# Performance work log

Hardware: AMD Instinct MI355X
Metric: run time of the kernel (lower is better)

The kernel has to match this reference:

```python
import jax, jax.numpy as jnp
import numpy as np

B, L, D = 2, 2048, 2048
H = 16
DH = D // H  # 128
EPS = 1e-6


def _rope_cos_sin(seq_len, dim, dtype):
    inv_freq = 1.0 / (10000.0 ** (jnp.arange(0, dim, 2, dtype=jnp.float32) / dim))
    t = jnp.arange(seq_len, dtype=jnp.float32)
    freqs = jnp.einsum('i,j->ij', t, inv_freq)          # [L, dim/2]
    emb = jnp.concatenate([freqs, freqs], axis=-1)      # [L, dim]
    return jnp.cos(emb).astype(dtype)[None, None], jnp.sin(emb).astype(dtype)[None, None]


def _rotate_half(x):
    x1, x2 = jnp.split(x, 2, axis=-1)
    return jnp.concatenate([-x2, x1], axis=-1)


def _rms_norm(x, w):
    var = jnp.mean(jnp.square(x), axis=-1, keepdims=True)
    return x * jax.lax.rsqrt(var + EPS) * w


def setup_inputs() -> dict:
    key = jax.random.key(0)
    ks = jax.random.split(key, 4)
    s_in = 1.0 / np.sqrt(D)
    return {
        'x': jax.random.normal(ks[0], (B, L, D), jnp.float32),
        'attention_mask': jnp.zeros((B, 1, 1, L), jnp.bool_),
        'Wqkv': jax.random.normal(ks[1], (D, 3 * D), jnp.float32) * s_in,
        'bqkv': jnp.zeros((3 * D,), jnp.float32),
        'Wout': jax.random.normal(ks[2], (D, D), jnp.float32) * s_in,
        'bout': jnp.zeros((D,), jnp.float32),
        'q_norm_w': jnp.ones((DH,), jnp.float32),
        'k_norm_w': jnp.ones((DH,), jnp.float32),
    }


def reference(x, attention_mask, Wqkv, bqkv, Wout, bout, q_norm_w, k_norm_w):
    b, l, d = x.shape
    qkv = x @ Wqkv + bqkv                                   # [B,L,3D]
    q, k, v = jnp.split(qkv, 3, axis=-1)
    # [B,H,L,DH]
    q = q.reshape(b, l, H, DH).transpose(0, 2, 1, 3)
    k = k.reshape(b, l, H, DH).transpose(0, 2, 1, 3)
    v = v.reshape(b, l, H, DH).transpose(0, 2, 1, 3)

    cos, sin = _rope_cos_sin(l, DH, x.dtype)
    q = q * cos + _rotate_half(q) * sin
    k = k * cos + _rotate_half(k) * sin

    q = _rms_norm(q, q_norm_w)
    k = _rms_norm(k, k_norm_w)

    # SDPA with additive (float-cast) mask, as in the original code
    scale = 1.0 / np.sqrt(DH)
    scores = jnp.einsum('bhqd,bhkd->bhqk', q, k) * scale
    scores = scores + attention_mask.astype(x.dtype)        # broadcast [B,1,1,L]
    attn = jax.nn.softmax(scores, axis=-1)
    out = jnp.einsum('bhqk,bhkd->bhqd', attn, v)            # [B,H,L,DH]

    # zero out masked query rows: padding_mask = mask.transpose(2,3) -> [B,1,L,1]
    padding_mask = jnp.swapaxes(attention_mask, 2, 3)
    out = jnp.where(padding_mask, 0.0, out)

    out = out.transpose(0, 2, 1, 3).reshape(b, l, d)
    return out @ Wout + bout
```

## Files before the change

kernel.cpp:

```cpp
#include <hip/hip_runtime.h>
#include <hip/hip_bf16.h>

typedef __bf16 bf16;
using bf16x8 = __attribute__((ext_vector_type(8))) __bf16;
using bf16x4 = __attribute__((ext_vector_type(4))) __bf16;
using f32x4  = __attribute__((ext_vector_type(4))) float;
using f32x16 = __attribute__((ext_vector_type(16))) float;

#define DEV __device__ __forceinline__

DEV void load_lds16(const void* g, void* l) {
  __builtin_amdgcn_global_load_lds(
      (const __attribute__((address_space(1))) void*)g,
      (__attribute__((address_space(3))) void*)l, 16, 0, 0);
}

__global__ void k_tab(float* __restrict__ invf) {
  int i = threadIdx.x;
  invf[i] = 1.0f / (float)pow(10000.0, (double)i / 64.0);
}

__global__ void k_f2b(const float* __restrict__ in, bf16* __restrict__ out, long n) {
  long i = ((long)blockIdx.x * blockDim.x + threadIdx.x) * 8;
  if (i >= n) return;
  float4 a = *(const float4*)(in + i);
  float4 b = *(const float4*)(in + i + 4);
  bf16x8 o;
  o[0] = (bf16)a.x; o[1] = (bf16)a.y; o[2] = (bf16)a.z; o[3] = (bf16)a.w;
  o[4] = (bf16)b.x; o[5] = (bf16)b.y; o[6] = (bf16)b.z; o[7] = (bf16)b.w;
  *(bf16x8*)(out + i) = o;
}

__global__ __launch_bounds__(256) void k_tconv(const float* __restrict__ in,
                                               bf16* __restrict__ out, int R, int C) {
  __shared__ float t[64][65];
  int nbc = C >> 6;
  long r0 = (long)(blockIdx.x / nbc) * 64, c0 = (long)(blockIdx.x % nbc) * 64;
  int tid = threadIdx.x;
#pragma unroll
  for (int i = 0; i < 4; ++i) {
    int ch = tid + i * 256;
    int r = ch >> 4, c4 = (ch & 15) * 4;
    float4 v = *(const float4*)(in + (r0 + r) * C + c0 + c4);
    t[r][c4] = v.x; t[r][c4 + 1] = v.y; t[r][c4 + 2] = v.z; t[r][c4 + 3] = v.w;
  }
  __syncthreads();
#pragma unroll
  for (int i = 0; i < 2; ++i) {
    int ch = tid + i * 256;
    int c = ch >> 3, r8 = (ch & 7) * 8;
    bf16x8 o;
#pragma unroll
    for (int j = 0; j < 8; ++j) o[j] = (bf16)t[r8 + j][c];
    *(bf16x8*)(out + (c0 + c) * R + r0 + r8) = o;
  }
}

template <typename OutT>
__global__ __launch_bounds__(256) void k_gemm_bt(
    const bf16* __restrict__ A, const bf16* __restrict__ Bt,
    const float* __restrict__ bias, OutT* __restrict__ C,
    int M, int N, int K, int fuse,
    const float* __restrict__ invf,
    const float* __restrict__ qw, const float* __restrict__ kw,
    bf16* __restrict__ q_r, bf16* __restrict__ k_r, bf16* __restrict__ v_t) {
  __shared__ __align__(16) bf16 lAB[2][128 * 64];
  bf16* lA = lAB[0];
  bf16* lB = lAB[1];
  int bid = blockIdx.x;
  if ((gridDim.x & 7) == 0) {
    int q = gridDim.x >> 3;
    bid = (bid & 7) * q + (bid >> 3);
  }
  int nbn = N >> 7;
  int bm = bid / nbn, bn = bid % nbn;
  const int tid = threadIdx.x, lane = tid & 63, wid = tid >> 6;
  const int wr = wid >> 1, wc = wid & 1;
  const int fr = lane & 15, fq = lane >> 4;
  const long abase = (long)bm * 128 * K, bbase = (long)bn * 128 * K;
  f32x4 acc[4][4] = {};

  for (int k0 = 0; k0 < K; k0 += 64) {
    __syncthreads();
#pragma unroll
    for (int it = 0; it < 4; ++it) {
      int ch = it * 256 + tid;
      int r = ch >> 3, u = ch & 7;
      load_lds16(A + abase + (long)r * K + k0 + ((u ^ (r & 7)) << 3), &lA[ch * 8]);
    }
#pragma unroll
    for (int it = 0; it < 4; ++it) {
      int ch = it * 256 + tid;
      int r = ch >> 3, u = ch & 7;
      load_lds16(Bt + bbase + (long)r * K + k0 + ((u ^ (r & 7)) << 3), &lB[ch * 8]);
    }
    __syncthreads();
    bf16x8 af[4][2], bf_[4][2];
#pragma unroll
    for (int m = 0; m < 4; ++m) {
      int R = wr * 64 + m * 16 + fr;
#pragma unroll
      for (int kk = 0; kk < 2; ++kk)
        af[m][kk] = *(const bf16x8*)&lA[R * 64 + (((kk * 4 + fq) ^ (R & 7)) << 3)];
    }
#pragma unroll
    for (int n = 0; n < 4; ++n) {
      int R = wc * 64 + n * 16 + fr;
#pragma unroll
      for (int kk = 0; kk < 2; ++kk)
        bf_[n][kk] = *(const bf16x8*)&lB[R * 64 + (((kk * 4 + fq) ^ (R & 7)) << 3)];
    }
#pragma unroll
    for (int m = 0; m < 4; ++m)
#pragma unroll
      for (int n = 0; n < 4; ++n)
#pragma unroll
        for (int kk = 0; kk < 2; ++kk)
          acc[m][n] = __builtin_amdgcn_mfma_f32_16x16x32_bf16(af[m][kk], bf_[n][kk],
                                                              acc[m][n], 0, 0, 0);
  }

  if (!fuse) {
#pragma unroll
    for (int n = 0; n < 4; ++n) {
      int col = bn * 128 + wc * 64 + n * 16 + fr;
      float bv = bias[col];
#pragma unroll
      for (int m = 0; m < 4; ++m) {
        int row0 = bm * 128 + wr * 64 + m * 16 + fq * 4;
#pragma unroll
        for (int r = 0; r < 4; ++r) {
          float v = acc[m][n][r] + bv;
          C[(long)(row0 + r) * N + col] = (OutT)v;
        }
      }
    }
    return;
  }

  __syncthreads();
  bf16* tile = lAB[0];
  const int h = bn & 15;
  const int b = bm >> 4, l0 = (bm & 15) << 7;

  if (bn < 32) {
#pragma unroll
    for (int n = 0; n < 4; ++n) {
      int col = wc * 64 + n * 16 + fr;
      float bv = bias[bn * 128 + col];
#pragma unroll
      for (int m = 0; m < 4; ++m)
#pragma unroll
        for (int r = 0; r < 4; ++r) {
          int row = wr * 64 + m * 16 + fq * 4 + r;
          tile[row * 128 + (col ^ ((row & 7) << 3))] = (bf16)(acc[m][n][r] + bv);
        }
    }
    __syncthreads();
    const float* wv = (bn < 16) ? qw : kw;
    bf16* dst0 = (bn < 16) ? q_r : k_r;
    const int tcol = tid & 15, rgrp = tid >> 4, i8 = tcol * 8;
    const bool lo = i8 < 64;
    float wvv[8], invv[8];
#pragma unroll
    for (int j = 0; j < 8; ++j) wvv[j] = wv[i8 + j];
#pragma unroll
    for (int j = 0; j < 8; ++j) invv[j] = invf[(i8 + j) & 63];
#pragma unroll
    for (int it = 0; it < 8; ++it) {
      int row = it * 16 + rgrp;
      float fl = (float)(l0 + row);
      float cc[8], sn[8];
#pragma unroll
      for (int j = 0; j < 8; ++j) __sincosf(fl * invv[j], &sn[j], &cc[j]);
      bf16x8 xv = *(const bf16x8*)&tile[row * 128 + (i8 ^ ((row & 7) << 3))];
      float v[8], p[8], rr[8];
      float ss = 0.f;
#pragma unroll
      for (int j = 0; j < 8; ++j) v[j] = (float)xv[j];
#pragma unroll
      for (int j = 0; j < 8; ++j) p[j] = __shfl_xor(v[j], 8);
#pragma unroll
      for (int j = 0; j < 8; ++j) {
        rr[j] = lo ? v[j] * cc[j] - p[j] * sn[j] : v[j] * cc[j] + p[j] * sn[j];
        ss += rr[j] * rr[j];
      }
      ss += __shfl_xor(ss, 1);
      ss += __shfl_xor(ss, 2);
      ss += __shfl_xor(ss, 4);
      ss += __shfl_xor(ss, 8);
      float inv = rsqrtf(ss * (1.f / 128.f) + 1e-6f);
      bf16x8 ov;
#pragma unroll
      for (int j = 0; j < 8; ++j) ov[j] = (bf16)(rr[j] * inv * wvv[j]);
      *(bf16x8*)(dst0 + ((long)((b * 16 + h) * 2048 + (l0 + row))) * 128 + i8) = ov;
    }
  } else {
#pragma unroll
    for (int n = 0; n < 4; ++n) {
      int col = wc * 64 + n * 16 + fr;
      float bv = bias[bn * 128 + col];
#pragma unroll
      for (int m = 0; m < 4; ++m)
#pragma unroll
        for (int r = 0; r < 4; ++r) {
          int row = wr * 64 + m * 16 + fq * 4 + r;
          tile[col * 128 + (row ^ ((col & 7) << 3))] = (bf16)(acc[m][n][r] + bv);
        }
    }
    __syncthreads();
    bf16* dstb = v_t + ((long)((b * 16 + h) * 128)) * 2048 + l0;
#pragma unroll
    for (int it = 0; it < 8; ++it) {
      int ch = it * 256 + tid;
      int d = ch >> 4, l8 = (ch & 15) * 8;
      bf16x8 vv = *(const bf16x8*)&tile[d * 128 + (l8 ^ ((d & 7) << 3))];
      *(bf16x8*)(dstb + (long)d * 2048 + l8) = vv;
    }
  }
}

__global__ __launch_bounds__(512, 2) void k_attn(
    const bf16* __restrict__ q_r, const bf16* __restrict__ k_r,
    const bf16* __restrict__ v_t, const unsigned char* __restrict__ amask,
    bf16* __restrict__ attno) {
  __shared__ __align__(16) bf16 lK[2][64 * 128];
  __shared__ __align__(16) bf16 lV[2][128 * 64];
  __shared__ int sAny;
  const int tid = threadIdx.x, lane = tid & 63, w = tid >> 6;
  const int hi = lane >> 5, q31 = lane & 31;
  const int bh = blockIdx.x & 31, qt = blockIdx.x >> 5;
  const int b = bh >> 4, h = bh & 15;
  const long hbase = (long)bh * 2048 * 128;
  const int q0 = qt * 256 + w * 32;
  const unsigned char* mb = amask + b * 2048;

  if (tid == 0) sAny = 0;
  __syncthreads();
  {
    unsigned mv = *(const unsigned*)(mb + tid * 4);
    if (mv) sAny = 1;
  }

  bf16x8 qf[8];
#pragma unroll
  for (int ksl = 0; ksl < 8; ++ksl)
    qf[ksl] = *(const bf16x8*)(q_r + hbase + (long)(q0 + q31) * 128 + ksl * 16 + hi * 8);

  f32x16 o[4] = {};
  float m_run = -1e30f, l_run = 0.f;
  const float SC2 = 0.08838834764831845f * 1.4426950408889634f;
  const float L2E = 1.4426950408889634f;

#define STAGE(buf, kv0)                                                              \
  {                                                                                  \
    _Pragma("unroll") for (int it = 0; it < 2; ++it) {                               \
      int g = it * 512 + w * 64 + lane;                                              \
      int r = g >> 4, u = g & 15;                                                    \
      load_lds16(k_r + hbase + (long)((kv0) + r) * 128 + ((u ^ (r & 7)) << 3),       \
                 &lK[buf][(it * 512 + w * 64) * 8]);                                 \
    }                                                                                \
    _Pragma("unroll") for (int it = 0; it < 2; ++it) {                               \
      int g = it * 512 + w * 64 + lane;                                              \
      int r = g >> 3, u = g & 7;                                                     \
      load_lds16(v_t + hbase + (long)r * 2048 + (kv0) + ((u ^ (r & 7)) << 3),        \
                 &lV[buf][(it * 512 + w * 64) * 8]);                                 \
    }                                                                                \
  }

  STAGE(0, 0);
  __syncthreads();
  const bool maskAny = sAny != 0;
  int cur = 0;
  for (int t = 0; t < 32; ++t) {
    const int kv0 = t << 6;
    if (t < 31) STAGE(cur ^ 1, kv0 + 64);

    f32x16 st0 = {}, st1 = {};
#pragma unroll
    for (int ksl = 0; ksl < 8; ++ksl) {
      const int u = ksl * 2 + hi;
      bf16x8 kf0 = *(const bf16x8*)&lK[cur][q31 * 128 + ((u ^ (q31 & 7)) << 3)];
      bf16x8 kf1 = *(const bf16x8*)&lK[cur][(32 + q31) * 128 + ((u ^ (q31 & 7)) << 3)];
      st0 = __builtin_amdgcn_mfma_f32_32x32x16_bf16(kf0, qf[ksl], st0, 0, 0, 0);
      st1 = __builtin_amdgcn_mfma_f32_32x32x16_bf16(kf1, qf[ksl], st1, 0, 0, 0);
    }

#pragma unroll
    for (int i = 0; i < 16; ++i) { st0[i] *= SC2; st1[i] *= SC2; }
    if (maskAny) {
#pragma unroll
      for (int i = 0; i < 16; ++i) {
        int c = (i & 3) + 8 * (i >> 2) + 4 * hi;
        if (mb[kv0 + c]) st0[i] += L2E;
        if (mb[kv0 + 32 + c]) st1[i] += L2E;
      }
    }

    float tm = st0[0];
#pragma unroll
    for (int i = 1; i < 16; ++i) tm = fmaxf(tm, st0[i]);
#pragma unroll
    for (int i = 0; i < 16; ++i) tm = fmaxf(tm, st1[i]);
    tm = fmaxf(tm, __shfl_xor(tm, 32));

    if (!__all(tm <= m_run + 8.f)) {
      float mn = fmaxf(m_run, tm);
      float corr = exp2f(m_run - mn);
      m_run = mn;
      l_run *= corr;
#pragma unroll
      for (int i = 0; i < 16; ++i) {
        float cr = __shfl(corr, (i & 3) + 8 * (i >> 2) + 4 * hi);
#pragma unroll
        for (int dt = 0; dt < 4; ++dt) o[dt][i] *= cr;
      }
    }

    float rs = 0.f;
#pragma unroll
    for (int i = 0; i < 16; ++i) { st0[i] = exp2f(st0[i] - m_run); rs += st0[i]; }
#pragma unroll
    for (int i = 0; i < 16; ++i) { st1[i] = exp2f(st1[i] - m_run); rs += st1[i]; }
    rs += __shfl_xor(rs, 32);
    l_run += rs;

    union UU { bf16x4 v; uint2 u; };
    union U8 { bf16x8 v; uint4 u; };
    bf16x8 pa[4];
#define MKPA(pidx, STX, bb)                                                          \
  {                                                                                  \
    UU plo, phi;                                                                     \
    plo.v = (bf16x4){(bf16)STX[bb], (bf16)STX[(bb) + 1], (bf16)STX[(bb) + 2],        \
                     (bf16)STX[(bb) + 3]};                                           \
    phi.v = (bf16x4){(bf16)STX[(bb) + 4], (bf16)STX[(bb) + 5], (bf16)STX[(bb) + 6],  \
                     (bf16)STX[(bb) + 7]};                                           \
    unsigned sx = hi ? plo.u.x : phi.u.x, sy = hi ? plo.u.y : phi.u.y;               \
    unsigned rx = (unsigned)__shfl_xor((int)sx, 32), ry = (unsigned)__shfl_xor((int)sy, 32); \
    U8 f;                                                                            \
    f.u.x = hi ? rx : plo.u.x; f.u.y = hi ? ry : plo.u.y;                            \
    f.u.z = hi ? phi.u.x : rx; f.u.w = hi ? phi.u.y : ry;                            \
    pa[pidx] = f.v;                                                                  \
  }
    MKPA(0, st0, 0) MKPA(1, st0, 8) MKPA(2, st1, 0) MKPA(3, st1, 8)
#undef MKPA

#pragma unroll
    for (int dt = 0; dt < 4; ++dt) {
      const int dr = dt * 32 + q31;
#pragma unroll
      for (int ks = 0; ks < 4; ++ks) {
        const int u = ks * 2 + hi;
        bf16x8 vb = *(const bf16x8*)&lV[cur][dr * 64 + ((u ^ (dr & 7)) << 3)];
        o[dt] = __builtin_amdgcn_mfma_f32_32x32x16_bf16(pa[ks], vb, o[dt], 0, 0, 0);
      }
    }

    __syncthreads();
    cur ^= 1;
  }
#undef STAGE

  float invl = 1.f / l_run;
#pragma unroll
  for (int i = 0; i < 16; ++i) {
    int q = (i & 3) + 8 * (i >> 2) + 4 * hi;
    int qrow = q0 + q;
    float inv = __shfl(invl, q);
    float zm = inv;
    if (maskAny) { if (mb[qrow]) zm = 0.f; }
#pragma unroll
    for (int dt = 0; dt < 4; ++dt)
      attno[(long)(b * 2048 + qrow) * 2048 + h * 128 + dt * 32 + q31] = (bf16)(o[dt][i] * zm);
  }
}

extern "C" void kernel_launch(void* const* d_in, const int* in_sizes, int n_in,
                              void* d_out, int out_size, void* d_ws, size_t ws_size,
                              hipStream_t stream) {
  const float* x = (const float*)d_in[0];
  const unsigned char* amask = (const unsigned char*)d_in[1];
  const float* Wqkv = (const float*)d_in[2];
  const float* bqkv = (const float*)d_in[3];
  const float* Wout = (const float*)d_in[4];
  const float* bout = (const float*)d_in[5];
  const float* qw = (const float*)d_in[6];
  const float* kw = (const float*)d_in[7];
  float* out = (float*)d_out;
  char* ws = (char*)d_ws;

  bf16* xb   = (bf16*)(ws);
  bf16* wqT  = (bf16*)(ws + 16777216);
  bf16* woT  = (bf16*)(ws + 41943040);
  bf16* q_r  = (bf16*)(ws + 100663296);
  bf16* k_r  = (bf16*)(ws + 117440512);
  bf16* v_t  = (bf16*)(ws + 134217728);
  float* invf = (float*)(ws + 150994944);
  bf16* attno = xb;

  k_tab<<<1, 64, 0, stream>>>(invf);
  k_f2b<<<4096, 256, 0, stream>>>(x, xb, 8388608L);
  k_tconv<<<32 * 96, 256, 0, stream>>>(Wqkv, wqT, 2048, 6144);
  k_tconv<<<32 * 32, 256, 0, stream>>>(Wout, woT, 2048, 2048);
  k_gemm_bt<bf16><<<32 * 48, 256, 0, stream>>>(xb, wqT, bqkv, (bf16*)nullptr,
                                               4096, 6144, 2048, 1,
                                               invf, qw, kw, q_r, k_r, v_t);
  k_attn<<<256, 512, 0, stream>>>(q_r, k_r, v_t, amask, attno);
  k_gemm_bt<float><<<32 * 16, 256, 0, stream>>>(attno, woT, bout, out,
                                                4096, 2048, 2048, 0,
                                                nullptr, nullptr, nullptr,
                                                nullptr, nullptr, nullptr);
}
```

Before: 309.3 us.

## Software-pipeline QK^T one tile ahead in attention and merge prep kernels

The attention loop now computes the next tile's QK^T scores while running softmax and PV on the current tile. It triple-buffers V in LDS and prefetches K/V two tiles ahead so the MFMA work of two stages can overlap. Launch bounds drop to one block per SM because LDS use grows, which may cut occupancy. Separately, the x cast, both weight transposes and the RoPE table kernels are merged into one launch to remove launch overhead.

```diff
diff --git a/kernel.cpp b/kernel.cpp
--- a/kernel.cpp
+++ b/kernel.cpp
@@ -15,28 +15,35 @@
       (__attribute__((address_space(3))) void*)l, 16, 0, 0);
 }
 
-__global__ void k_tab(float* __restrict__ invf) {
-  int i = threadIdx.x;
-  invf[i] = 1.0f / (float)pow(10000.0, (double)i / 64.0);
-}
-
-__global__ void k_f2b(const float* __restrict__ in, bf16* __restrict__ out, long n) {
-  long i = ((long)blockIdx.x * blockDim.x + threadIdx.x) * 8;
-  if (i >= n) return;
-  float4 a = *(const float4*)(in + i);
-  float4 b = *(const float4*)(in + i + 4);
-  bf16x8 o;
-  o[0] = (bf16)a.x; o[1] = (bf16)a.y; o[2] = (bf16)a.z; o[3] = (bf16)a.w;
-  o[4] = (bf16)b.x; o[5] = (bf16)b.y; o[6] = (bf16)b.z; o[7] = (bf16)b.w;
-  *(bf16x8*)(out + i) = o;
-}
-
-__global__ __launch_bounds__(256) void k_tconv(const float* __restrict__ in,
-                                               bf16* __restrict__ out, int R, int C) {
+__global__ __launch_bounds__(256) void k_prep(
+    const float* __restrict__ x, bf16* __restrict__ xb,
+    const float* __restrict__ Wq, bf16* __restrict__ wqT,
+    const float* __restrict__ Wo, bf16* __restrict__ woT,
+    float* __restrict__ invf) {
   __shared__ float t[64][65];
+  int bid = blockIdx.x;
+  int tid = threadIdx.x;
+  if (bid < 4096) {
+    long i = ((long)bid * 256 + tid) * 8;
+    float4 a = *(const float4*)(x + i);
+    float4 b = *(const float4*)(x + i + 4);
+    bf16x8 o;
+    o[0] = (bf16)a.x; o[1] = (bf16)a.y; o[2] = (bf16)a.z; o[3] = (bf16)a.w;
+    o[4] = (bf16)b.x; o[5] = (bf16)b.y; o[6] = (bf16)b.z; o[7] = (bf16)b.w;
+    *(bf16x8*)(xb + i) = o;
+    return;
+  }
+  if (bid >= 8192) {
+    if (tid < 64) invf[tid] = 1.0f / (float)pow(10000.0, (double)tid / 64.0);
+    return;
+  }
+  const float* in;
+  bf16* out;
+  int R, C, rb;
+  if (bid < 7168) { in = Wq; out = wqT; R = 2048; C = 6144; rb = bid - 4096; }
+  else            { in = Wo; out = woT; R = 2048; C = 2048; rb = bid - 7168; }
   int nbc = C >> 6;
-  long r0 = (long)(blockIdx.x / nbc) * 64, c0 = (long)(blockIdx.x % nbc) * 64;
-  int tid = threadIdx.x;
+  long r0 = (long)(rb / nbc) * 64, c0 = (long)(rb % nbc) * 64;
 #pragma unroll
   for (int i = 0; i < 4; ++i) {
     int ch = tid + i * 256;
@@ -220,12 +227,12 @@
   }
 }
 
-__global__ __launch_bounds__(512, 2) void k_attn(
+__global__ __launch_bounds__(512, 1) void k_attn(
     const bf16* __restrict__ q_r, const bf16* __restrict__ k_r,
     const bf16* __restrict__ v_t, const unsigned char* __restrict__ amask,
     bf16* __restrict__ attno) {
   __shared__ __align__(16) bf16 lK[2][64 * 128];
-  __shared__ __align__(16) bf16 lV[2][128 * 64];
+  __shared__ __align__(16) bf16 lV[3][128 * 64];
   __shared__ int sAny;
   const int tid = threadIdx.x, lane = tid & 63, w = tid >> 6;
   const int hi = lane >> 5, q31 = lane & 31;
@@ -252,7 +259,7 @@
   const float SC2 = 0.08838834764831845f * 1.4426950408889634f;
   const float L2E = 1.4426950408889634f;
 
-#define STAGE(buf, kv0)                                                              \
+#define STAGE_K(buf, kv0)                                                            \
   {                                                                                  \
     _Pragma("unroll") for (int it = 0; it < 2; ++it) {                               \
       int g = it * 512 + w * 64 + lane;                                              \
@@ -260,6 +267,9 @@
       load_lds16(k_r + hbase + (long)((kv0) + r) * 128 + ((u ^ (r & 7)) << 3),       \
                  &lK[buf][(it * 512 + w * 64) * 8]);                                 \
     }                                                                                \
+  }
+#define STAGE_V(buf, kv0)                                                            \
+  {                                                                                  \
     _Pragma("unroll") for (int it = 0; it < 2; ++it) {                               \
       int g = it * 512 + w * 64 + lane;                                              \
       int r = g >> 3, u = g & 7;                                                     \
@@ -268,22 +278,39 @@
     }                                                                                \
   }
 
-  STAGE(0, 0);
+  STAGE_K(0, 0) STAGE_V(0, 0) STAGE_K(1, 64) STAGE_V(1, 64)
   __syncthreads();
   const bool maskAny = sAny != 0;
-  int cur = 0;
+
+  f32x16 st0 = {}, st1 = {};
+#pragma unroll
+  for (int ksl = 0; ksl < 8; ++ksl) {
+    const int u = ksl * 2 + hi;
+    bf16x8 kf0 = *(const bf16x8*)&lK[0][q31 * 128 + ((u ^ (q31 & 7)) << 3)];
+    bf16x8 kf1 = *(const bf16x8*)&lK[0][(32 + q31) * 128 + ((u ^ (q31 & 7)) << 3)];
+    st0 = __builtin_amdgcn_mfma_f32_32x32x16_bf16(kf0, qf[ksl], st0, 0, 0, 0);
+    st1 = __builtin_amdgcn_mfma_f32_32x32x16_bf16(kf1, qf[ksl], st1, 0, 0, 0);
+  }
+  __syncthreads();
+
   for (int t = 0; t < 32; ++t) {
     const int kv0 = t << 6;
-    if (t < 31) STAGE(cur ^ 1, kv0 + 64);
-
-    f32x16 st0 = {}, st1 = {};
-#pragma unroll
-    for (int ksl = 0; ksl < 8; ++ksl) {
-      const int u = ksl * 2 + hi;
-      bf16x8 kf0 = *(const bf16x8*)&lK[cur][q31 * 128 + ((u ^ (q31 & 7)) << 3)];
-      bf16x8 kf1 = *(const bf16x8*)&lK[cur][(32 + q31) * 128 + ((u ^ (q31 & 7)) << 3)];
-      st0 = __builtin_amdgcn_mfma_f32_32x32x16_bf16(kf0, qf[ksl], st0, 0, 0, 0);
-      st1 = __builtin_amdgcn_mfma_f32_32x32x16_bf16(kf1, qf[ksl], st1, 0, 0, 0);
+    if (t + 2 < 32) {
+      STAGE_K(t & 1, kv0 + 128)
+      STAGE_V((t + 2) % 3, kv0 + 128)
+    }
+
+    f32x16 sn0 = {}, sn1 = {};
+    if (t < 31) {
+      const bf16* kb = lK[(t + 1) & 1];
+#pragma unroll
+      for (int ksl = 0; ksl < 8; ++ksl) {
+        const int u = ksl * 2 + hi;
+        bf16x8 kf0 = *(const bf16x8*)&kb[q31 * 128 + ((u ^ (q31 & 7)) << 3)];
+        bf16x8 kf1 = *(const bf16x8*)&kb[(32 + q31) * 128 + ((u ^ (q31 & 7)) << 3)];
+        sn0 = __builtin_amdgcn_mfma_f32_32x32x16_bf16(kf0, qf[ksl], sn0, 0, 0, 0);
+        sn1 = __builtin_amdgcn_mfma_f32_32x32x16_bf16(kf1, qf[ksl], sn1, 0, 0, 0);
+      }
     }
 
 #pragma unroll
@@ -296,7 +323,6 @@
         if (mb[kv0 + 32 + c]) st1[i] += L2E;
       }
     }
-
     float tm = st0[0];
 #pragma unroll
     for (int i = 1; i < 16; ++i) tm = fmaxf(tm, st0[i]);
@@ -345,21 +371,24 @@
     MKPA(0, st0, 0) MKPA(1, st0, 8) MKPA(2, st1, 0) MKPA(3, st1, 8)
 #undef MKPA
 
+    const bf16* vb3 = lV[t % 3];
 #pragma unroll
     for (int dt = 0; dt < 4; ++dt) {
       const int dr = dt * 32 + q31;
 #pragma unroll
       for (int ks = 0; ks < 4; ++ks) {
         const int u = ks * 2 + hi;
-        bf16x8 vb = *(const bf16x8*)&lV[cur][dr * 64 + ((u ^ (dr & 7)) << 3)];
+        bf16x8 vb = *(const bf16x8*)&vb3[dr * 64 + ((u ^ (dr & 7)) << 3)];
         o[dt] = __builtin_amdgcn_mfma_f32_32x32x16_bf16(pa[ks], vb, o[dt], 0, 0, 0);
       }
     }
 
     __syncthreads();
-    cur ^= 1;
-  }
-#undef STAGE
+    st0 = sn0;
+    st1 = sn1;
+  }
+#undef STAGE_K
+#undef STAGE_V
 
   float invl = 1.f / l_run;
 #pragma unroll
@@ -398,10 +427,7 @@
   float* invf = (float*)(ws + 150994944);
   bf16* attno = xb;
 
-  k_tab<<<1, 64, 0, stream>>>(invf);
-  k_f2b<<<4096, 256, 0, stream>>>(x, xb, 8388608L);
-  k_tconv<<<32 * 96, 256, 0, stream>>>(Wqkv, wqT, 2048, 6144);
-  k_tconv<<<32 * 32, 256, 0, stream>>>(Wout, woT, 2048, 2048);
+  k_prep<<<8193, 256, 0, stream>>>(x, xb, Wqkv, wqT, Wout, woT, invf);
   k_gemm_bt<bf16><<<32 * 48, 256, 0, stream>>>(xb, wqT, bqkv, (bf16*)nullptr,
                                                4096, 6144, 2048, 1,
                                                invf, qw, kw, q_r, k_r, v_t);
```

New measurement: 304.2 us. About the same (-1.6%).
